# Performance work log

Measured on AMD Instinct MI355X. Metric: run time of the kernel, lower is better.

## Reference

```python
import jax, jax.numpy as jnp
import numpy as np

B, S, H, F, E, TOPK = 2, 2048, 1024, 2048, 8, 2


def setup_inputs() -> dict:
    key = jax.random.key(0)
    k1, k2, k3, k4, k5 = jax.random.split(key, 5)
    scale_h = 1.0 / np.sqrt(H)
    scale_f = 1.0 / np.sqrt(F)
    return {
        "hidden_states": jax.random.normal(k1, (B, S, H), dtype=jnp.float32),
        "gate_w": jax.random.normal(k2, (E, H), dtype=jnp.float32) * scale_h,
        "w1": jax.random.normal(k3, (E, F, H), dtype=jnp.float32) * scale_h,
        "w2": jax.random.normal(k4, (E, H, F), dtype=jnp.float32) * scale_f,
        "w3": jax.random.normal(k5, (E, F, H), dtype=jnp.float32) * scale_h,
    }


def reference(hidden_states, gate_w, w1, w2, w3):
    b, s, h = hidden_states.shape
    x = hidden_states.reshape(-1, h)                      # [T, H]
    T = x.shape[0]
    router_logits = x @ gate_w.T                          # [T, E]
    probs = jax.nn.softmax(router_logits.astype(jnp.float32), axis=-1)
    rw, sel = jax.lax.top_k(probs, TOPK)                  # [T, k]
    rw = rw / jnp.sum(rw, axis=-1, keepdims=True)
    rw = rw.astype(x.dtype)
    # combine weights [T, E]: routing weight where selected, else 0
    combine = jnp.zeros((T, E), dtype=x.dtype).at[
        jnp.arange(T)[:, None], sel].add(rw)
    # dense dispatch: compute every expert on all tokens, mask via combine
    h1 = jnp.einsum('th,efh->etf', x, w1)                 # [E, T, F]
    h3 = jnp.einsum('th,efh->etf', x, w3)
    gated = jax.nn.silu(h1) * h3
    out_e = jnp.einsum('etf,ehf->eth', gated, w2)         # [E, T, H]
    final = jnp.einsum('eth,te->th', out_e, combine)      # [T, H]
    return final.reshape(b, s, h), router_logits
```

## Files before the change

### kernel.cpp

```cpp
#include <hip/hip_runtime.h>
#include <hip/hip_bf16.h>

#define TT 4096
#define HH 1024
#define FF 2048
#define EE 8
#define NCONV 8192

typedef short short8_t __attribute__((ext_vector_type(8)));
typedef float f32x4 __attribute__((ext_vector_type(4)));

__device__ __forceinline__ unsigned short f2b(float f) {
  union { float f; unsigned u; } v; v.f = f;
  return (unsigned short)((v.u + 0x7fffu + ((v.u >> 16) & 1u)) >> 16);
}

__device__ __forceinline__ short8_t pack8(float4 a, float4 b) {
  short8_t r;
  r[0] = (short)f2b(a.x); r[1] = (short)f2b(a.y);
  r[2] = (short)f2b(a.z); r[3] = (short)f2b(a.w);
  r[4] = (short)f2b(b.x); r[5] = (short)f2b(b.y);
  r[6] = (short)f2b(b.z); r[7] = (short)f2b(b.w);
  return r;
}

__device__ __forceinline__ void gload16(const unsigned short* g, unsigned short* l) {
  __builtin_amdgcn_global_load_lds(
      (const __attribute__((address_space(1))) void*)g,
      (__attribute__((address_space(3))) void*)l, 16, 0, 0);
}

__device__ __forceinline__ void conv_body(const float* __restrict__ src,
                                          unsigned short* __restrict__ dst,
                                          int b, int tid) {
  size_t i = ((size_t)b * 256 + tid) * 8;
  float4 a = *reinterpret_cast<const float4*>(src + i);
  float4 c = *reinterpret_cast<const float4*>(src + i + 4);
  *reinterpret_cast<short8_t*>(dst + i) = pack8(a, c);
}

__global__ __launch_bounds__(256) void front_kernel(
    const float* __restrict__ x, const float* __restrict__ gw,
    const float* __restrict__ w1, const float* __restrict__ w3,
    const float* __restrict__ w2,
    float* __restrict__ out_logits, float* __restrict__ final_out,
    unsigned short* __restrict__ xbf,
    unsigned short* __restrict__ w1bf, unsigned short* __restrict__ w3bf,
    unsigned short* __restrict__ w2bf, int do_w2,
    int* __restrict__ sel01, float2* __restrict__ w01)
{
  int tid = threadIdx.x;
  int b = blockIdx.x;
  if (b >= TT) {
    int cb = b - TT;
    if (cb < NCONV)          conv_body(w1, w1bf, cb, tid);
    else if (cb < 2 * NCONV) conv_body(w3, w3bf, cb - NCONV, tid);
    else                     conv_body(w2, w2bf, cb - 2 * NCONV, tid);
    return;
  }
  int t = b;

  __shared__ float xs[HH];
  __shared__ float lg[EE];

  float4 v = reinterpret_cast<const float4*>(x + (size_t)t * HH)[tid];
  xs[tid * 4 + 0] = v.x; xs[tid * 4 + 1] = v.y;
  xs[tid * 4 + 2] = v.z; xs[tid * 4 + 3] = v.w;
  ushort4 b4;
  b4.x = f2b(v.x); b4.y = f2b(v.y); b4.z = f2b(v.z); b4.w = f2b(v.w);
  reinterpret_cast<ushort4*>(xbf + (size_t)t * HH)[tid] = b4;
  float4 z4; z4.x = z4.y = z4.z = z4.w = 0.f;
  reinterpret_cast<float4*>(final_out + (size_t)t * HH)[tid] = z4;
  __syncthreads();

  int lane = tid & 63, wv = tid >> 6;
  for (int e = wv; e < EE; e += 4) {
    float s = 0.f;
    const float* g = gw + (size_t)e * HH;
#pragma unroll
    for (int j = 0; j < HH / 64; ++j) s += xs[lane + j * 64] * g[lane + j * 64];
#pragma unroll
    for (int off = 32; off > 0; off >>= 1) s += __shfl_down(s, off);
    if (lane == 0) lg[e] = s;
  }
  __syncthreads();

  if (tid < 8) out_logits[(size_t)t * EE + tid] = lg[tid];
  if (tid == 0) {
    float l[EE];
#pragma unroll
    for (int e = 0; e < EE; ++e) l[e] = lg[e];
    int e0 = 0;
#pragma unroll
    for (int e = 1; e < EE; ++e) if (l[e] > l[e0]) e0 = e;
    int e1 = -1;
#pragma unroll
    for (int e = 0; e < EE; ++e) if (e != e0 && (e1 < 0 || l[e] > l[e1])) e1 = e;
    float p1 = expf(l[e1] - l[e0]);
    float w0 = 1.f / (1.f + p1);
    float w1v = p1 * w0;
    sel01[t] = e0 | (e1 << 8);
    w01[t] = make_float2(w0, w1v);
  }
}

__global__ __launch_bounds__(256) void build_kernel(
    const int* __restrict__ sel01, const float2* __restrict__ w01,
    int* __restrict__ counts, int* __restrict__ tokidx, float* __restrict__ rww)
{
  int e = blockIdx.x;
  int tid = threadIdx.x, lane = tid & 63, wv = tid >> 6;
  __shared__ int wsum[4];
  int base = 0;
  for (int t0 = 0; t0 < TT; t0 += 256) {
    int t = t0 + tid;
    int s = sel01[t];
    int e0 = s & 255, e1 = (s >> 8) & 255;
    bool hit = (e0 == e) || (e1 == e);
    float w = 0.f;
    if (hit) { float2 ww = w01[t]; w = (e0 == e) ? ww.x : ww.y; }
    unsigned long long m = __ballot(hit);
    int wpre = __popcll(m & ((1ull << lane) - 1));
    if (lane == 63) wsum[wv] = wpre + (hit ? 1 : 0);
    __syncthreads();
    int wbase = base;
    for (int q = 0; q < wv; ++q) wbase += wsum[q];
    if (hit) {
      int pos = wbase + wpre;
      tokidx[e * TT + pos] = t;
      rww[e * TT + pos] = w;
    }
    base += wsum[0] + wsum[1] + wsum[2] + wsum[3];
    __syncthreads();
  }
  if (tid == 0) counts[e] = base;
}

__global__ __launch_bounds__(256) void conv_kernel(
    const float* __restrict__ src, unsigned short* __restrict__ dst)
{
  conv_body(src, dst, blockIdx.x, threadIdx.x);
}

__global__ __launch_bounds__(256) void up_gate_kernel(
    const unsigned short* __restrict__ xbf,
    const unsigned short* __restrict__ w1bf, const unsigned short* __restrict__ w3bf,
    const int* __restrict__ counts, const int* __restrict__ tokidx,
    unsigned short* __restrict__ gated)
{
  int e = blockIdx.z;
  int n = counts[e];
  int row0 = blockIdx.y * 128;
  if (row0 >= n) return;
  int fbase = blockIdx.x * 64;

  int pe = 0;
  for (int q = 0; q < e; ++q) pe += (counts[q] + 127) & ~127;

  __shared__ unsigned short As[3][128 * 32];
  __shared__ unsigned short B1s[3][64 * 32];
  __shared__ unsigned short B3s[3][64 * 32];

  int tid = threadIdx.x;
  int lane = tid & 63, wv = tid >> 6;
  int srow = wv * 16 + (lane >> 2);
  int skoff = (lane & 3) * 8;

  int r0 = min(row0 + srow, n - 1);
  int r1 = min(row0 + 64 + srow, n - 1);
  int t0 = tokidx[e * TT + r0];
  int t1 = tokidx[e * TT + r1];
  const unsigned short* ga0 = xbf + (size_t)t0 * HH + skoff;
  const unsigned short* ga1 = xbf + (size_t)t1 * HH + skoff;
  const unsigned short* gb1 = w1bf + ((size_t)e * FF + fbase + srow) * HH + skoff;
  const unsigned short* gb3 = w3bf + ((size_t)e * FF + fbase + srow) * HH + skoff;

#define STAGE_UG(tt, bb) do { int kk = (tt) * 32;            \
    gload16(ga0 + kk, &As[bb][wv * 512]);                    \
    gload16(ga1 + kk, &As[bb][2048 + wv * 512]);             \
    gload16(gb1 + kk, &B1s[bb][wv * 512]);                   \
    gload16(gb3 + kk, &B3s[bb][wv * 512]); } while (0)

  int wr = (wv >> 1) * 64, wc = (wv & 1) * 32;
  int fr = lane & 15, fk = (lane >> 4) * 8;

  f32x4 acc1[4][2], acc3[4][2];
#pragma unroll
  for (int m = 0; m < 4; ++m)
#pragma unroll
    for (int nn = 0; nn < 2; ++nn) { acc1[m][nn] = (f32x4)0.f; acc3[m][nn] = (f32x4)0.f; }

  const int NK = HH / 32;
  STAGE_UG(0, 0);
  STAGE_UG(1, 1);

  for (int t = 0; t < NK; ++t) {
    if (t < NK - 1) asm volatile("s_waitcnt vmcnt(4)" ::: "memory");
    else            asm volatile("s_waitcnt vmcnt(0)" ::: "memory");
    __builtin_amdgcn_s_barrier();
    __builtin_amdgcn_sched_barrier(0);
    if (t + 2 < NK) STAGE_UG(t + 2, (t + 2) % 3);
    int cb = t % 3;

    short8_t a[4], b1f[2], b3f[2];
#pragma unroll
    for (int m = 0; m < 4; ++m)
      a[m] = *reinterpret_cast<const short8_t*>(&As[cb][(wr + m * 16 + fr) * 32 + fk]);
#pragma unroll
    for (int nn = 0; nn < 2; ++nn) {
      b1f[nn] = *reinterpret_cast<const short8_t*>(&B1s[cb][(wc + nn * 16 + fr) * 32 + fk]);
      b3f[nn] = *reinterpret_cast<const short8_t*>(&B3s[cb][(wc + nn * 16 + fr) * 32 + fk]);
    }
#pragma unroll
    for (int m = 0; m < 4; ++m)
#pragma unroll
      for (int nn = 0; nn < 2; ++nn) {
        acc1[m][nn] = __builtin_amdgcn_mfma_f32_16x16x32_bf16(a[m], b1f[nn], acc1[m][nn], 0, 0, 0);
        acc3[m][nn] = __builtin_amdgcn_mfma_f32_16x16x32_bf16(a[m], b3f[nn], acc3[m][nn], 0, 0, 0);
      }
  }
#undef STAGE_UG

  size_t gbase = ((size_t)pe + row0) * FF + fbase;
#pragma unroll
  for (int m = 0; m < 4; ++m) {
#pragma unroll
    for (int nn = 0; nn < 2; ++nn) {
      f32x4 h1v = acc1[m][nn], h3v = acc3[m][nn];
#pragma unroll
      for (int j = 0; j < 4; ++j) {
        float z = h1v[j];
        float val = (z / (1.f + expf(-z))) * h3v[j];
        int r = wr + m * 16 + (lane >> 4) * 4 + j;
        int c = wc + nn * 16 + fr;
        gated[gbase + (size_t)r * FF + c] = f2b(val);
      }
    }
  }
}

__global__ __launch_bounds__(256) void down_kernel(
    const unsigned short* __restrict__ gated,
    const unsigned short* __restrict__ w2bf,
    const int* __restrict__ counts, const int* __restrict__ tokidx,
    const float* __restrict__ rww,
    float* __restrict__ final_out)
{
  int e = blockIdx.z;
  int n = counts[e];
  int row0 = blockIdx.y * 128;
  if (row0 >= n) return;
  int hbase = blockIdx.x * 128;
  int valid = min(128, n - row0);

  int pe = 0;
  for (int q = 0; q < e; ++q) pe += (counts[q] + 127) & ~127;

  __shared__ unsigned short As[3][128 * 32];
  __shared__ unsigned short Bs[3][128 * 32];

  int tid = threadIdx.x;
  int lane = tid & 63, wv = tid >> 6;
  int srow = wv * 16 + (lane >> 2);
  int skoff = (lane & 3) * 8;

  const unsigned short* ga0 = gated + ((size_t)pe + row0 + srow) * FF + skoff;
  const unsigned short* ga1 = ga0 + (size_t)64 * FF;
  const unsigned short* gb0 = w2bf + ((size_t)e * HH + hbase + srow) * FF + skoff;
  const unsigned short* gb1 = gb0 + (size_t)64 * FF;

#define STAGE_DN(tt, bb) do { int kk = (tt) * 32;            \
    gload16(ga0 + kk, &As[bb][wv * 512]);                    \
    gload16(ga1 + kk, &As[bb][2048 + wv * 512]);             \
    gload16(gb0 + kk, &Bs[bb][wv * 512]);                    \
    gload16(gb1 + kk, &Bs[bb][2048 + wv * 512]); } while (0)

  int wr = (wv >> 1) * 64, wc = (wv & 1) * 64;
  int fr = lane & 15, fk = (lane >> 4) * 8;

  f32x4 acc[4][4];
#pragma unroll
  for (int m = 0; m < 4; ++m)
#pragma unroll
    for (int nn = 0; nn < 4; ++nn) acc[m][nn] = (f32x4)0.f;

  const int NK = FF / 32;
  STAGE_DN(0, 0);
  STAGE_DN(1, 1);

  for (int t = 0; t < NK; ++t) {
    if (t < NK - 1) asm volatile("s_waitcnt vmcnt(4)" ::: "memory");
    else            asm volatile("s_waitcnt vmcnt(0)" ::: "memory");
    __builtin_amdgcn_s_barrier();
    __builtin_amdgcn_sched_barrier(0);
    if (t + 2 < NK) STAGE_DN(t + 2, (t + 2) % 3);
    int cb = t % 3;

    short8_t a[4], bf[4];
#pragma unroll
    for (int m = 0; m < 4; ++m)
      a[m] = *reinterpret_cast<const short8_t*>(&As[cb][(wr + m * 16 + fr) * 32 + fk]);
#pragma unroll
    for (int nn = 0; nn < 4; ++nn)
      bf[nn] = *reinterpret_cast<const short8_t*>(&Bs[cb][(wc + nn * 16 + fr) * 32 + fk]);
#pragma unroll
    for (int m = 0; m < 4; ++m)
#pragma unroll
      for (int nn = 0; nn < 4; ++nn)
        acc[m][nn] = __builtin_amdgcn_mfma_f32_16x16x32_bf16(a[m], bf[nn], acc[m][nn], 0, 0, 0);
  }
#undef STAGE_DN

#pragma unroll
  for (int m = 0; m < 4; ++m) {
    int rbase = wr + m * 16 + (lane >> 4) * 4;
#pragma unroll
    for (int j = 0; j < 4; ++j) {
      int r = rbase + j;
      if (r < valid) {
        int t = tokidx[e * TT + row0 + r];
        float w = rww[e * TT + row0 + r];
#pragma unroll
        for (int nn = 0; nn < 4; ++nn) {
          int c = hbase + wc + nn * 16 + fr;
          atomicAdd(&final_out[(size_t)t * HH + c], w * acc[m][nn][j]);
        }
      }
    }
  }
}

extern "C" void kernel_launch(void* const* d_in, const int* in_sizes, int n_in,
                              void* d_out, int out_size, void* d_ws, size_t ws_size,
                              hipStream_t stream) {
  const float* x  = (const float*)d_in[0];
  const float* gw = (const float*)d_in[1];
  const float* w1 = (const float*)d_in[2];
  const float* w2 = (const float*)d_in[3];
  const float* w3 = (const float*)d_in[4];

  float* final_out  = (float*)d_out;
  float* out_logits = final_out + (size_t)TT * HH;

  char* ws = (char*)d_ws;
  int*    counts = (int*)(ws + 0);
  int*    sel01  = (int*)(ws + 1024);
  float2* w01    = (float2*)(ws + 20480);
  int*    tokidx = (int*)(ws + 53248);
  float*  rww    = (float*)(ws + 184320);
  unsigned short* xbf   = (unsigned short*)(ws + 315392);
  unsigned short* w1bf  = (unsigned short*)(ws + 8704000);
  unsigned short* w3bf  = (unsigned short*)(ws + 42258432);
  unsigned short* gated = (unsigned short*)(ws + 75812864);
  const size_t base_end = 113561600;
  bool big = ws_size >= base_end + 33554432;
  unsigned short* w2bf = big ? (unsigned short*)(ws + base_end) : w1bf;

  int nconvs = big ? 3 : 2;
  front_kernel<<<TT + nconvs * NCONV, 256, 0, stream>>>(
      x, gw, w1, w3, w2, out_logits, final_out, xbf, w1bf, w3bf, w2bf,
      big ? 1 : 0, sel01, w01);
  build_kernel<<<EE, 256, 0, stream>>>(sel01, w01, counts, tokidx, rww);
  up_gate_kernel<<<dim3(FF / 64, TT / 128, EE), 256, 0, stream>>>(
      xbf, w1bf, w3bf, counts, tokidx, gated);
  if (!big) conv_kernel<<<NCONV, 256, 0, stream>>>(w2, w1bf);
  down_kernel<<<dim3(HH / 128, TT / 128, EE), 256, 0, stream>>>(
      gated, w2bf, counts, tokidx, rww, final_out);
}
```

Baseline: 265.5 us.

## Grid-stride weight conversion blocks and unroll triple-buffered GEMM loops by three

The front kernel now launches a fixed 3072 conversion blocks that grid-stride over all weight chunks, instead of one block per chunk. This is meant to cut block-launch overhead and tail effects. The up-gate and down GEMM K-loops are manually unrolled by three, so the triple-buffer indices are compile-time constants, which removes the modulo arithmetic and dynamic LDS address computation. This grows code size, and the hand-written tail steps must keep the vmcnt accounting correct.

After: 314.4 us. 18.4% more time.

```diff
diff --git a/kernel.cpp b/kernel.cpp
--- a/kernel.cpp
+++ b/kernel.cpp
@@ -6,6 +6,7 @@
 #define FF 2048
 #define EE 8
 #define NCONV 8192
+#define CONVB 3072
 
 typedef short short8_t __attribute__((ext_vector_type(8)));
 typedef float f32x4 __attribute__((ext_vector_type(4)));
@@ -53,9 +54,12 @@
   int b = blockIdx.x;
   if (b >= TT) {
     int cb = b - TT;
-    if (cb < NCONV)          conv_body(w1, w1bf, cb, tid);
-    else if (cb < 2 * NCONV) conv_body(w3, w3bf, cb - NCONV, tid);
-    else                     conv_body(w2, w2bf, cb - 2 * NCONV, tid);
+    int total = do_w2 ? 3 * NCONV : 2 * NCONV;
+    for (int w = cb; w < total; w += CONVB) {
+      if (w < NCONV)          conv_body(w1, w1bf, w, tid);
+      else if (w < 2 * NCONV) conv_body(w3, w3bf, w - NCONV, tid);
+      else                    conv_body(w2, w2bf, w - 2 * NCONV, tid);
+    }
     return;
   }
   int t = b;
@@ -175,12 +179,6 @@
   const unsigned short* gb1 = w1bf + ((size_t)e * FF + fbase + srow) * HH + skoff;
   const unsigned short* gb3 = w3bf + ((size_t)e * FF + fbase + srow) * HH + skoff;
 
-#define STAGE_UG(tt, bb) do { int kk = (tt) * 32;            \
-    gload16(ga0 + kk, &As[bb][wv * 512]);                    \
-    gload16(ga1 + kk, &As[bb][2048 + wv * 512]);             \
-    gload16(gb1 + kk, &B1s[bb][wv * 512]);                   \
-    gload16(gb3 + kk, &B3s[bb][wv * 512]); } while (0)
-
   int wr = (wv >> 1) * 64, wc = (wv & 1) * 32;
   int fr = lane & 15, fk = (lane >> 4) * 8;
 
@@ -190,36 +188,45 @@
 #pragma unroll
     for (int nn = 0; nn < 2; ++nn) { acc1[m][nn] = (f32x4)0.f; acc3[m][nn] = (f32x4)0.f; }
 
-  const int NK = HH / 32;
-  STAGE_UG(0, 0);
-  STAGE_UG(1, 1);
-
-  for (int t = 0; t < NK; ++t) {
-    if (t < NK - 1) asm volatile("s_waitcnt vmcnt(4)" ::: "memory");
-    else            asm volatile("s_waitcnt vmcnt(0)" ::: "memory");
-    __builtin_amdgcn_s_barrier();
-    __builtin_amdgcn_sched_barrier(0);
-    if (t + 2 < NK) STAGE_UG(t + 2, (t + 2) % 3);
-    int cb = t % 3;
-
-    short8_t a[4], b1f[2], b3f[2];
-#pragma unroll
-    for (int m = 0; m < 4; ++m)
-      a[m] = *reinterpret_cast<const short8_t*>(&As[cb][(wr + m * 16 + fr) * 32 + fk]);
-#pragma unroll
-    for (int nn = 0; nn < 2; ++nn) {
-      b1f[nn] = *reinterpret_cast<const short8_t*>(&B1s[cb][(wc + nn * 16 + fr) * 32 + fk]);
-      b3f[nn] = *reinterpret_cast<const short8_t*>(&B3s[cb][(wc + nn * 16 + fr) * 32 + fk]);
-    }
-#pragma unroll
-    for (int m = 0; m < 4; ++m)
-#pragma unroll
-      for (int nn = 0; nn < 2; ++nn) {
-        acc1[m][nn] = __builtin_amdgcn_mfma_f32_16x16x32_bf16(a[m], b1f[nn], acc1[m][nn], 0, 0, 0);
-        acc3[m][nn] = __builtin_amdgcn_mfma_f32_16x16x32_bf16(a[m], b3f[nn], acc3[m][nn], 0, 0, 0);
-      }
-  }
-#undef STAGE_UG
+#define UG_STAGE(KK, BB) do {                                  \
+    gload16(ga0 + (KK), &As[BB][wv * 512]);                    \
+    gload16(ga1 + (KK), &As[BB][2048 + wv * 512]);             \
+    gload16(gb1 + (KK), &B1s[BB][wv * 512]);                   \
+    gload16(gb3 + (KK), &B3s[BB][wv * 512]); } while (0)
+
+#define UG_COMPUTE(CB) do {                                                                   \
+    short8_t a[4], b1f[2], b3f[2];                                                            \
+    _Pragma("unroll") for (int m = 0; m < 4; ++m)                                             \
+      a[m] = *reinterpret_cast<const short8_t*>(&As[CB][(wr + m * 16 + fr) * 32 + fk]);       \
+    _Pragma("unroll") for (int nn = 0; nn < 2; ++nn) {                                        \
+      b1f[nn] = *reinterpret_cast<const short8_t*>(&B1s[CB][(wc + nn * 16 + fr) * 32 + fk]);  \
+      b3f[nn] = *reinterpret_cast<const short8_t*>(&B3s[CB][(wc + nn * 16 + fr) * 32 + fk]);  \
+    }                                                                                         \
+    _Pragma("unroll") for (int m = 0; m < 4; ++m)                                             \
+      _Pragma("unroll") for (int nn = 0; nn < 2; ++nn) {                                      \
+        acc1[m][nn] = __builtin_amdgcn_mfma_f32_16x16x32_bf16(a[m], b1f[nn], acc1[m][nn], 0, 0, 0); \
+        acc3[m][nn] = __builtin_amdgcn_mfma_f32_16x16x32_bf16(a[m], b3f[nn], acc3[m][nn], 0, 0, 0); \
+      } } while (0)
+
+#define UG_STEP(CB, SB, TCUR, DOSTAGE, WAITN) do {             \
+    asm volatile("s_waitcnt vmcnt(" #WAITN ")" ::: "memory");  \
+    __builtin_amdgcn_s_barrier();                              \
+    __builtin_amdgcn_sched_barrier(0);                         \
+    if (DOSTAGE) UG_STAGE(((TCUR) + 2) * 32, SB);              \
+    UG_COMPUTE(CB); } while (0)
+
+  UG_STAGE(0, 0);
+  UG_STAGE(32, 1);
+  for (int tb = 0; tb < 30; tb += 3) {
+    UG_STEP(0, 2, tb + 0, 1, 4);
+    UG_STEP(1, 0, tb + 1, 1, 4);
+    UG_STEP(2, 1, tb + 2, 1, 4);
+  }
+  UG_STEP(0, 2, 30, 0, 4);
+  UG_STEP(1, 0, 31, 0, 0);
+#undef UG_STAGE
+#undef UG_COMPUTE
+#undef UG_STEP
 
   size_t gbase = ((size_t)pe + row0) * FF + fbase;
 #pragma unroll
@@ -269,12 +276,6 @@
   const unsigned short* gb0 = w2bf + ((size_t)e * HH + hbase + srow) * FF + skoff;
   const unsigned short* gb1 = gb0 + (size_t)64 * FF;
 
-#define STAGE_DN(tt, bb) do { int kk = (tt) * 32;            \
-    gload16(ga0 + kk, &As[bb][wv * 512]);                    \
-    gload16(ga1 + kk, &As[bb][2048 + wv * 512]);             \
-    gload16(gb0 + kk, &Bs[bb][wv * 512]);                    \
-    gload16(gb1 + kk, &Bs[bb][2048 + wv * 512]); } while (0)
-
   int wr = (wv >> 1) * 64, wc = (wv & 1) * 64;
   int fr = lane & 15, fk = (lane >> 4) * 8;
 
@@ -284,32 +285,44 @@
 #pragma unroll
     for (int nn = 0; nn < 4; ++nn) acc[m][nn] = (f32x4)0.f;
 
-  const int NK = FF / 32;
-  STAGE_DN(0, 0);
-  STAGE_DN(1, 1);
-
-  for (int t = 0; t < NK; ++t) {
-    if (t < NK - 1) asm volatile("s_waitcnt vmcnt(4)" ::: "memory");
-    else            asm volatile("s_waitcnt vmcnt(0)" ::: "memory");
-    __builtin_amdgcn_s_barrier();
-    __builtin_amdgcn_sched_barrier(0);
-    if (t + 2 < NK) STAGE_DN(t + 2, (t + 2) % 3);
-    int cb = t % 3;
-
-    short8_t a[4], bf[4];
-#pragma unroll
-    for (int m = 0; m < 4; ++m)
-      a[m] = *reinterpret_cast<const short8_t*>(&As[cb][(wr + m * 16 + fr) * 32 + fk]);
-#pragma unroll
-    for (int nn = 0; nn < 4; ++nn)
-      bf[nn] = *reinterpret_cast<const short8_t*>(&Bs[cb][(wc + nn * 16 + fr) * 32 + fk]);
-#pragma unroll
-    for (int m = 0; m < 4; ++m)
-#pragma unroll
-      for (int nn = 0; nn < 4; ++nn)
-        acc[m][nn] = __builtin_amdgcn_mfma_f32_16x16x32_bf16(a[m], bf[nn], acc[m][nn], 0, 0, 0);
-  }
-#undef STAGE_DN
+#define DN_STAGE(KK, BB) do {                                  \
+    gload16(ga0 + (KK), &As[BB][wv * 512]);                    \
+    gload16(ga1 + (KK), &As[BB][2048 + wv * 512]);             \
+    gload16(gb0 + (KK), &Bs[BB][wv * 512]);                    \
+    gload16(gb1 + (KK), &Bs[BB][2048 + wv * 512]); } while (0)
+
+#define DN_COMPUTE(CB) do {                                                                  \
+    short8_t a[4], bf[4];                                                                    \
+    _Pragma("unroll") for (int m = 0; m < 4; ++m)                                            \
+      a[m] = *reinterpret_cast<const short8_t*>(&As[CB][(wr + m * 16 + fr) * 32 + fk]);      \
+    _Pragma("unroll") for (int nn = 0; nn < 4; ++nn)                                         \
+      bf[nn] = *reinterpret_cast<const short8_t*>(&Bs[CB][(wc + nn * 16 + fr) * 32 + fk]);   \
+    _Pragma("unroll") for (int m = 0; m < 4; ++m)                                            \
+      _Pragma("unroll") for (int nn = 0; nn < 4; ++nn)                                       \
+        acc[m][nn] = __builtin_amdgcn_mfma_f32_16x16x32_bf16(a[m], bf[nn], acc[m][nn], 0, 0, 0); \
+  } while (0)
+
+#define DN_STEP(CB, SB, TCUR, DOSTAGE, WAITN) do {             \
+    asm volatile("s_waitcnt vmcnt(" #WAITN ")" ::: "memory");  \
+    __builtin_amdgcn_s_barrier();                              \
+    __builtin_amdgcn_sched_barrier(0);                         \
+    if (DOSTAGE) DN_STAGE(((TCUR) + 2) * 32, SB);              \
+    DN_COMPUTE(CB); } while (0)
+
+  DN_STAGE(0, 0);
+  DN_STAGE(32, 1);
+  for (int tb = 0; tb < 60; tb += 3) {
+    DN_STEP(0, 2, tb + 0, 1, 4);
+    DN_STEP(1, 0, tb + 1, 1, 4);
+    DN_STEP(2, 1, tb + 2, 1, 4);
+  }
+  DN_STEP(0, 2, 60, 1, 4);
+  DN_STEP(1, 0, 61, 1, 4);
+  DN_STEP(2, 1, 62, 0, 4);
+  DN_STEP(0, 1, 63, 0, 0);
+#undef DN_STAGE
+#undef DN_COMPUTE
+#undef DN_STEP
 
 #pragma unroll
   for (int m = 0; m < 4; ++m) {
@@ -356,8 +369,7 @@
   bool big = ws_size >= base_end + 33554432;
   unsigned short* w2bf = big ? (unsigned short*)(ws + base_end) : w1bf;
 
-  int nconvs = big ? 3 : 2;
-  front_kernel<<<TT + nconvs * NCONV, 256, 0, stream>>>(
+  front_kernel<<<TT + CONVB, 256, 0, stream>>>(
       x, gw, w1, w3, w2, out_logits, final_out, xbf, w1bf, w3bf, w2bf,
       big ? 1 : 0, sel01, w01);
   build_kernel<<<EE, 256, 0, stream>>>(sel01, w01, counts, tokidx, rww);
```

## Switch GEMM pipelines to double buffering and batch weight conversion loads

Applied to the files above, without the earlier changes.

Both the up/gate and down GEMM kernels go from a 3-stage LDS ring with explicit vmcnt waits to a simpler 2-buffer scheme with __syncthreads, cutting LDS use, which may raise occupancy. In exchange each iteration now waits for all outstanding loads, so prefetch depth drops. The fp32-to-bf16 weight conversion now has each thread issue 8 independent float4 loads before converting, using fewer, larger blocks to raise memory-level parallelism.

After: 266.2 us. About the same (+0.3%).

```diff
diff --git a/kernel.cpp b/kernel.cpp
--- a/kernel.cpp
+++ b/kernel.cpp
@@ -5,7 +5,7 @@
 #define HH 1024
 #define FF 2048
 #define EE 8
-#define NCONV 8192
+#define NC32 2048
 
 typedef short short8_t __attribute__((ext_vector_type(8)));
 typedef float f32x4 __attribute__((ext_vector_type(4)));
@@ -13,15 +13,6 @@
 __device__ __forceinline__ unsigned short f2b(float f) {
   union { float f; unsigned u; } v; v.f = f;
   return (unsigned short)((v.u + 0x7fffu + ((v.u >> 16) & 1u)) >> 16);
-}
-
-__device__ __forceinline__ short8_t pack8(float4 a, float4 b) {
-  short8_t r;
-  r[0] = (short)f2b(a.x); r[1] = (short)f2b(a.y);
-  r[2] = (short)f2b(a.z); r[3] = (short)f2b(a.w);
-  r[4] = (short)f2b(b.x); r[5] = (short)f2b(b.y);
-  r[6] = (short)f2b(b.z); r[7] = (short)f2b(b.w);
-  return r;
 }
 
 __device__ __forceinline__ void gload16(const unsigned short* g, unsigned short* l) {
@@ -30,13 +21,20 @@
       (__attribute__((address_space(3))) void*)l, 16, 0, 0);
 }
 
-__device__ __forceinline__ void conv_body(const float* __restrict__ src,
-                                          unsigned short* __restrict__ dst,
-                                          int b, int tid) {
-  size_t i = ((size_t)b * 256 + tid) * 8;
-  float4 a = *reinterpret_cast<const float4*>(src + i);
-  float4 c = *reinterpret_cast<const float4*>(src + i + 4);
-  *reinterpret_cast<short8_t*>(dst + i) = pack8(a, c);
+__device__ __forceinline__ void conv_ilp(const float* __restrict__ src,
+                                         unsigned short* __restrict__ dst,
+                                         int c, int tid) {
+  size_t base = (size_t)c * 8192 + tid * 4;
+  float4 v[8];
+#pragma unroll
+  for (int j = 0; j < 8; ++j)
+    v[j] = *reinterpret_cast<const float4*>(src + base + j * 1024);
+#pragma unroll
+  for (int j = 0; j < 8; ++j) {
+    ushort4 b4;
+    b4.x = f2b(v[j].x); b4.y = f2b(v[j].y); b4.z = f2b(v[j].z); b4.w = f2b(v[j].w);
+    *reinterpret_cast<ushort4*>(dst + base + j * 1024) = b4;
+  }
 }
 
 __global__ __launch_bounds__(256) void front_kernel(
@@ -46,16 +44,16 @@
     float* __restrict__ out_logits, float* __restrict__ final_out,
     unsigned short* __restrict__ xbf,
     unsigned short* __restrict__ w1bf, unsigned short* __restrict__ w3bf,
-    unsigned short* __restrict__ w2bf, int do_w2,
+    unsigned short* __restrict__ w2bf,
     int* __restrict__ sel01, float2* __restrict__ w01)
 {
   int tid = threadIdx.x;
   int b = blockIdx.x;
   if (b >= TT) {
     int cb = b - TT;
-    if (cb < NCONV)          conv_body(w1, w1bf, cb, tid);
-    else if (cb < 2 * NCONV) conv_body(w3, w3bf, cb - NCONV, tid);
-    else                     conv_body(w2, w2bf, cb - 2 * NCONV, tid);
+    if (cb < NC32)          conv_ilp(w1, w1bf, cb, tid);
+    else if (cb < 2 * NC32) conv_ilp(w3, w3bf, cb - NC32, tid);
+    else                    conv_ilp(w2, w2bf, cb - 2 * NC32, tid);
     return;
   }
   int t = b;
@@ -139,7 +137,7 @@
 __global__ __launch_bounds__(256) void conv_kernel(
     const float* __restrict__ src, unsigned short* __restrict__ dst)
 {
-  conv_body(src, dst, blockIdx.x, threadIdx.x);
+  conv_ilp(src, dst, blockIdx.x, threadIdx.x);
 }
 
 __global__ __launch_bounds__(256) void up_gate_kernel(
@@ -157,9 +155,9 @@
   int pe = 0;
   for (int q = 0; q < e; ++q) pe += (counts[q] + 127) & ~127;
 
-  __shared__ unsigned short As[3][128 * 32];
-  __shared__ unsigned short B1s[3][64 * 32];
-  __shared__ unsigned short B3s[3][64 * 32];
+  __shared__ unsigned short As[2][128 * 32];
+  __shared__ unsigned short B1s[2][64 * 32];
+  __shared__ unsigned short B3s[2][64 * 32];
 
   int tid = threadIdx.x;
   int lane = tid & 63, wv = tid >> 6;
@@ -175,12 +173,6 @@
   const unsigned short* gb1 = w1bf + ((size_t)e * FF + fbase + srow) * HH + skoff;
   const unsigned short* gb3 = w3bf + ((size_t)e * FF + fbase + srow) * HH + skoff;
 
-#define STAGE_UG(tt, bb) do { int kk = (tt) * 32;            \
-    gload16(ga0 + kk, &As[bb][wv * 512]);                    \
-    gload16(ga1 + kk, &As[bb][2048 + wv * 512]);             \
-    gload16(gb1 + kk, &B1s[bb][wv * 512]);                   \
-    gload16(gb3 + kk, &B3s[bb][wv * 512]); } while (0)
-
   int wr = (wv >> 1) * 64, wc = (wv & 1) * 32;
   int fr = lane & 15, fk = (lane >> 4) * 8;
 
@@ -190,26 +182,30 @@
 #pragma unroll
     for (int nn = 0; nn < 2; ++nn) { acc1[m][nn] = (f32x4)0.f; acc3[m][nn] = (f32x4)0.f; }
 
-  const int NK = HH / 32;
-  STAGE_UG(0, 0);
-  STAGE_UG(1, 1);
-
-  for (int t = 0; t < NK; ++t) {
-    if (t < NK - 1) asm volatile("s_waitcnt vmcnt(4)" ::: "memory");
-    else            asm volatile("s_waitcnt vmcnt(0)" ::: "memory");
-    __builtin_amdgcn_s_barrier();
-    __builtin_amdgcn_sched_barrier(0);
-    if (t + 2 < NK) STAGE_UG(t + 2, (t + 2) % 3);
-    int cb = t % 3;
+  gload16(ga0, &As[0][wv * 512]);
+  gload16(ga1, &As[0][2048 + wv * 512]);
+  gload16(gb1, &B1s[0][wv * 512]);
+  gload16(gb3, &B3s[0][wv * 512]);
+
+  int cur = 0;
+  for (int k0 = 0; k0 < HH; k0 += 32) {
+    __syncthreads();
+    if (k0 + 32 < HH) {
+      int nxt = cur ^ 1, kn = k0 + 32;
+      gload16(ga0 + kn, &As[nxt][wv * 512]);
+      gload16(ga1 + kn, &As[nxt][2048 + wv * 512]);
+      gload16(gb1 + kn, &B1s[nxt][wv * 512]);
+      gload16(gb3 + kn, &B3s[nxt][wv * 512]);
+    }
 
     short8_t a[4], b1f[2], b3f[2];
 #pragma unroll
     for (int m = 0; m < 4; ++m)
-      a[m] = *reinterpret_cast<const short8_t*>(&As[cb][(wr + m * 16 + fr) * 32 + fk]);
+      a[m] = *reinterpret_cast<const short8_t*>(&As[cur][(wr + m * 16 + fr) * 32 + fk]);
 #pragma unroll
     for (int nn = 0; nn < 2; ++nn) {
-      b1f[nn] = *reinterpret_cast<const short8_t*>(&B1s[cb][(wc + nn * 16 + fr) * 32 + fk]);
-      b3f[nn] = *reinterpret_cast<const short8_t*>(&B3s[cb][(wc + nn * 16 + fr) * 32 + fk]);
+      b1f[nn] = *reinterpret_cast<const short8_t*>(&B1s[cur][(wc + nn * 16 + fr) * 32 + fk]);
+      b3f[nn] = *reinterpret_cast<const short8_t*>(&B3s[cur][(wc + nn * 16 + fr) * 32 + fk]);
     }
 #pragma unroll
     for (int m = 0; m < 4; ++m)
@@ -218,8 +214,8 @@
         acc1[m][nn] = __builtin_amdgcn_mfma_f32_16x16x32_bf16(a[m], b1f[nn], acc1[m][nn], 0, 0, 0);
         acc3[m][nn] = __builtin_amdgcn_mfma_f32_16x16x32_bf16(a[m], b3f[nn], acc3[m][nn], 0, 0, 0);
       }
-  }
-#undef STAGE_UG
+    cur ^= 1;
+  }
 
   size_t gbase = ((size_t)pe + row0) * FF + fbase;
 #pragma unroll
@@ -256,8 +252,8 @@
   int pe = 0;
   for (int q = 0; q < e; ++q) pe += (counts[q] + 127) & ~127;
 
-  __shared__ unsigned short As[3][128 * 32];
-  __shared__ unsigned short Bs[3][128 * 32];
+  __shared__ unsigned short As[2][128 * 32];
+  __shared__ unsigned short Bs[2][128 * 32];
 
   int tid = threadIdx.x;
   int lane = tid & 63, wv = tid >> 6;
@@ -269,12 +265,6 @@
   const unsigned short* gb0 = w2bf + ((size_t)e * HH + hbase + srow) * FF + skoff;
   const unsigned short* gb1 = gb0 + (size_t)64 * FF;
 
-#define STAGE_DN(tt, bb) do { int kk = (tt) * 32;            \
-    gload16(ga0 + kk, &As[bb][wv * 512]);                    \
-    gload16(ga1 + kk, &As[bb][2048 + wv * 512]);             \
-    gload16(gb0 + kk, &Bs[bb][wv * 512]);                    \
-    gload16(gb1 + kk, &Bs[bb][2048 + wv * 512]); } while (0)
-
   int wr = (wv >> 1) * 64, wc = (wv & 1) * 64;
   int fr = lane & 15, fk = (lane >> 4) * 8;
 
@@ -284,32 +274,36 @@
 #pragma unroll
     for (int nn = 0; nn < 4; ++nn) acc[m][nn] = (f32x4)0.f;
 
-  const int NK = FF / 32;
-  STAGE_DN(0, 0);
-  STAGE_DN(1, 1);
-
-  for (int t = 0; t < NK; ++t) {
-    if (t < NK - 1) asm volatile("s_waitcnt vmcnt(4)" ::: "memory");
-    else            asm volatile("s_waitcnt vmcnt(0)" ::: "memory");
-    __builtin_amdgcn_s_barrier();
-    __builtin_amdgcn_sched_barrier(0);
-    if (t + 2 < NK) STAGE_DN(t + 2, (t + 2) % 3);
-    int cb = t % 3;
+  gload16(ga0, &As[0][wv * 512]);
+  gload16(ga1, &As[0][2048 + wv * 512]);
+  gload16(gb0, &Bs[0][wv * 512]);
+  gload16(gb1, &Bs[0][2048 + wv * 512]);
+
+  int cur = 0;
+  for (int k0 = 0; k0 < FF; k0 += 32) {
+    __syncthreads();
+    if (k0 + 32 < FF) {
+      int nxt = cur ^ 1, kn = k0 + 32;
+      gload16(ga0 + kn, &As[nxt][wv * 512]);
+      gload16(ga1 + kn, &As[nxt][2048 + wv * 512]);
+      gload16(gb0 + kn, &Bs[nxt][wv * 512]);
+      gload16(gb1 + kn, &Bs[nxt][2048 + wv * 512]);
+    }
 
     short8_t a[4], bf[4];
 #pragma unroll
     for (int m = 0; m < 4; ++m)
-      a[m] = *reinterpret_cast<const short8_t*>(&As[cb][(wr + m * 16 + fr) * 32 + fk]);
+      a[m] = *reinterpret_cast<const short8_t*>(&As[cur][(wr + m * 16 + fr) * 32 + fk]);
 #pragma unroll
     for (int nn = 0; nn < 4; ++nn)
-      bf[nn] = *reinterpret_cast<const short8_t*>(&Bs[cb][(wc + nn * 16 + fr) * 32 + fk]);
+      bf[nn] = *reinterpret_cast<const short8_t*>(&Bs[cur][(wc + nn * 16 + fr) * 32 + fk]);
 #pragma unroll
     for (int m = 0; m < 4; ++m)
 #pragma unroll
       for (int nn = 0; nn < 4; ++nn)
         acc[m][nn] = __builtin_amdgcn_mfma_f32_16x16x32_bf16(a[m], bf[nn], acc[m][nn], 0, 0, 0);
-  }
-#undef STAGE_DN
+    cur ^= 1;
+  }
 
 #pragma unroll
   for (int m = 0; m < 4; ++m) {
@@ -356,14 +350,14 @@
   bool big = ws_size >= base_end + 33554432;
   unsigned short* w2bf = big ? (unsigned short*)(ws + base_end) : w1bf;
 
-  int nconvs = big ? 3 : 2;
-  front_kernel<<<TT + nconvs * NCONV, 256, 0, stream>>>(
+  int nconvblk = (big ? 3 : 2) * NC32;
+  front_kernel<<<TT + nconvblk, 256, 0, stream>>>(
       x, gw, w1, w3, w2, out_logits, final_out, xbf, w1bf, w3bf, w2bf,
-      big ? 1 : 0, sel01, w01);
+      sel01, w01);
   build_kernel<<<EE, 256, 0, stream>>>(sel01, w01, counts, tokidx, rww);
   up_gate_kernel<<<dim3(FF / 64, TT / 128, EE), 256, 0, stream>>>(
       xbf, w1bf, w3bf, counts, tokidx, gated);
-  if (!big) conv_kernel<<<NCONV, 256, 0, stream>>>(w2, w1bf);
+  if (!big) conv_kernel<<<NC32, 256, 0, stream>>>(w2, w1bf);
   down_kernel<<<dim3(HH / 128, TT / 128, EE), 256, 0, stream>>>(
       gated, w2bf, counts, tokidx, rww, final_out);
 }
```
